# Kernel optimization log

Measured on AMD Instinct MI355X. Metric: run time of the kernel, lower is better.

The kernel has to match this reference:

```python
import jax, jax.numpy as jnp
import numpy as np

N_NODES = 100000
N_EDGES = 3200000
N_GRAPHS = 2000
IN_DIM = 12
HID = 48
ADME = 20
EPS = 1e-5


def setup_inputs() -> dict:
    key = jax.random.key(0)
    ks = jax.random.split(key, 24)
    x = jax.random.normal(ks[0], (N_NODES, IN_DIM), jnp.float32)
    edge_index = jax.random.randint(ks[1], (2, N_EDGES), 0, N_NODES, dtype=jnp.int64)
    batch = jnp.sort(jax.random.randint(ks[2], (N_NODES,), 0, N_GRAPHS, dtype=jnp.int64))
    adme = jax.random.normal(ks[3], (N_GRAPHS, ADME), jnp.float32)

    def lin(k, fo, fi):
        bound = 1.0 / np.sqrt(fi)
        return jax.random.uniform(k, (fo, fi), jnp.float32, -bound, bound)

    params = {
        # SAGEConv layer 0: lin_l (neighbors, with bias) and lin_r (root)
        'wl0': lin(ks[4], HID, IN_DIM), 'wr0': lin(ks[5], HID, IN_DIM),
        'bc0': jnp.zeros((HID,), jnp.float32),
        'g0': jnp.ones((HID,), jnp.float32), 'be0': jnp.zeros((HID,), jnp.float32),
        # SAGEConv layer 1
        'wl1': lin(ks[6], HID, HID), 'wr1': lin(ks[7], HID, HID),
        'bc1': jnp.zeros((HID,), jnp.float32),
        'g1': jnp.ones((HID,), jnp.float32), 'be1': jnp.zeros((HID,), jnp.float32),
        # head: Linear(116,64) -> BN -> ReLU -> Linear(64,32) -> ReLU -> Linear(32,1)
        'hw1': lin(ks[8], 64, 2 * HID + ADME), 'hb1': jnp.zeros((64,), jnp.float32),
        'hg1': jnp.ones((64,), jnp.float32), 'hbe1': jnp.zeros((64,), jnp.float32),
        'hw2': lin(ks[9], 32, 64), 'hb2': jnp.zeros((32,), jnp.float32),
        'hw3': lin(ks[10], 1, 32), 'hb3': jnp.zeros((1,), jnp.float32),
    }
    return dict(x=x, edge_index=edge_index, batch=batch, adme=adme, **params)


def _sage(x, src, dst, wl, wr, b):
    # mean-aggregate source features at destination nodes, then two linears
    msum = jax.ops.segment_sum(x[src], dst, num_segments=N_NODES)
    cnt = jax.ops.segment_sum(jnp.ones((src.shape[0],), x.dtype), dst, num_segments=N_NODES)
    agg = msum / jnp.maximum(cnt, 1.0)[:, None]
    return agg @ wl.T + x @ wr.T + b


def _bn(x, g, b):
    m = x.mean(0)
    v = x.var(0)  # biased variance (BatchNorm training-mode math)
    return g * (x - m) * jax.lax.rsqrt(v + EPS) + b


def reference(x, edge_index, batch, adme,
              wl0, wr0, bc0, g0, be0,
              wl1, wr1, bc1, g1, be1,
              hw1, hb1, hg1, hbe1, hw2, hb2, hw3, hb3):
    src, dst = edge_index[0], edge_index[1]
    # backbone (dropout is identity in eval)
    h = jax.nn.relu(_bn(_sage(x, src, dst, wl0, wr0, bc0), g0, be0))
    h = jax.nn.relu(_bn(_sage(h, src, dst, wl1, wr1, bc1), g1, be1))
    # global mean / max pools over graph ids
    s = jax.ops.segment_sum(h, batch, num_segments=N_GRAPHS)
    n = jax.ops.segment_sum(jnp.ones((h.shape[0],), h.dtype), batch, num_segments=N_GRAPHS)
    mean_p = s / jnp.maximum(n, 1.0)[:, None]
    max_p = jax.ops.segment_max(h, batch, num_segments=N_GRAPHS)
    max_p = jnp.where(n[:, None] > 0, max_p, 0.0)
    combined = jnp.concatenate([mean_p, max_p, adme], axis=-1)  # [B, 116]
    z = jax.nn.relu(_bn(combined @ hw1.T + hb1, hg1, hbe1))
    z = jax.nn.relu(z @ hw2.T + hb2)
    return (z @ hw3.T + hb3)[:, 0]
```

## Files before the change

kernel.cpp:

```cpp
#include <hip/hip_runtime.h>

#define NNODES  100000
#define NEDGES  3200000
#define NGRAPHS 2000
#define INDIM   12
#define HID     48
#define CEPS    1e-5f
#define CAP     96
#define SRCMID  (NNODES / 2)

#define BSHIFT   8
#define NBUCKET  ((NNODES + 255) / 256)
#define CAPB     8704
#define P1_BLOCKS 125
#define P1_EDGES (NEDGES / P1_BLOCKS)

#define SCAN_CHUNK 1024
#define NSCAN_BLOCKS ((NNODES + SCAN_CHUNK - 1) / SCAN_CHUNK)

__device__ inline void f4add(float4& a, const float4 b) {
  a.x += b.x; a.y += b.y; a.z += b.z; a.w += b.w;
}
__device__ inline float blo(unsigned u) { return __uint_as_float(u << 16); }
__device__ inline float bhi(unsigned u) { return __uint_as_float(u & 0xffff0000u); }
__device__ inline unsigned bpack(float a, float b) {
  unsigned ua = __float_as_uint(a), ub = __float_as_uint(b);
  ua = (ua + 0x7fffu + ((ua >> 16) & 1u)) >> 16;
  ub = (ub + 0x7fffu + ((ub >> 16) & 1u)) >> 16;
  return ua | (ub << 16);
}

__global__ __launch_bounds__(256) void convert_x_kernel(
    const float* __restrict__ x, uint4* __restrict__ xb) {
  int idx = blockIdx.x * blockDim.x + threadIdx.x;
  if (idx >= NNODES * INDIM / 8) return;
  const float4* p = (const float4*)(x + (size_t)idx * 8);
  float4 v0 = p[0], v1 = p[1];
  uint4 o;
  o.x = bpack(v0.x, v0.y); o.y = bpack(v0.z, v0.w);
  o.z = bpack(v1.x, v1.y); o.w = bpack(v1.z, v1.w);
  xb[idx] = o;
}

__global__ __launch_bounds__(256) void bucket_p1_kernel(
    const int* __restrict__ ei, int* __restrict__ bucket_cursor,
    unsigned int* __restrict__ bucketed) {
  __shared__ int hist[NBUCKET];
  __shared__ int lcur[NBUCKET];
  for (int b = threadIdx.x; b < NBUCKET; b += 256) hist[b] = 0;
  __syncthreads();
  const int base = blockIdx.x * P1_EDGES;
  for (int off = threadIdx.x * 4; off < P1_EDGES; off += 1024) {
    int4 d4 = *(const int4*)(ei + NEDGES + base + off);
    atomicAdd(&hist[(d4.x >> BSHIFT) % NBUCKET], 1);
    atomicAdd(&hist[(d4.y >> BSHIFT) % NBUCKET], 1);
    atomicAdd(&hist[(d4.z >> BSHIFT) % NBUCKET], 1);
    atomicAdd(&hist[(d4.w >> BSHIFT) % NBUCKET], 1);
  }
  __syncthreads();
  for (int b = threadIdx.x; b < NBUCKET; b += 256)
    lcur[b] = atomicAdd(&bucket_cursor[b], hist[b]);
  __syncthreads();
  for (int off = threadIdx.x * 4; off < P1_EDGES; off += 1024) {
    int4 s4 = *(const int4*)(ei + base + off);
    int4 d4 = *(const int4*)(ei + NEDGES + base + off);
    {
      int b0 = (d4.x >> BSHIFT) % NBUCKET; int p = atomicAdd(&lcur[b0], 1);
      if ((unsigned)p < (unsigned)CAPB)
        bucketed[(size_t)b0 * CAPB + p] = ((unsigned)(d4.x & 255) << 24) | ((unsigned)s4.x & 0xFFFFFFu);
    }
    {
      int b1 = (d4.y >> BSHIFT) % NBUCKET; int p = atomicAdd(&lcur[b1], 1);
      if ((unsigned)p < (unsigned)CAPB)
        bucketed[(size_t)b1 * CAPB + p] = ((unsigned)(d4.y & 255) << 24) | ((unsigned)s4.y & 0xFFFFFFu);
    }
    {
      int b2 = (d4.z >> BSHIFT) % NBUCKET; int p = atomicAdd(&lcur[b2], 1);
      if ((unsigned)p < (unsigned)CAPB)
        bucketed[(size_t)b2 * CAPB + p] = ((unsigned)(d4.z & 255) << 24) | ((unsigned)s4.z & 0xFFFFFFu);
    }
    {
      int b3 = (d4.w >> BSHIFT) % NBUCKET; int p = atomicAdd(&lcur[b3], 1);
      if ((unsigned)p < (unsigned)CAPB)
        bucketed[(size_t)b3 * CAPB + p] = ((unsigned)(d4.w & 255) << 24) | ((unsigned)s4.w & 0xFFFFFFu);
    }
  }
}

__global__ __launch_bounds__(256) void fill_p2_kernel(
    const unsigned int* __restrict__ bucketed, const int* __restrict__ bucket_cursor,
    int* __restrict__ slots, int* __restrict__ cnt) {
  __shared__ int clo[256], chi[256];
  clo[threadIdx.x] = 0; chi[threadIdx.x] = 0;
  __syncthreads();
  int b = blockIdx.x;
  int count = bucket_cursor[b];
  if (count > CAPB) count = CAPB;
  size_t bb = (size_t)b * CAPB;
  for (int i = threadIdx.x; i < count; i += 256) {
    unsigned v = bucketed[bb + i];
    int dl = (int)(v >> 24);
    int s = (int)(v & 0xFFFFFFu);
    int node = b * 256 + dl;
    if (node < NNODES) {
      if (s < SRCMID) {
        int p = atomicAdd(&clo[dl], 1);
        if ((unsigned)p < (unsigned)CAP) slots[(size_t)node * CAP + p] = s;
      } else {
        int p = atomicAdd(&chi[dl], 1);
        if ((unsigned)p < (unsigned)CAP) slots[(size_t)node * CAP + (CAP - 1 - p)] = s;
      }
    }
  }
  __syncthreads();
  int node = b * 256 + threadIdx.x;
  if (node < NNODES)
    cnt[node] = min(clo[threadIdx.x], CAP) | (min(chi[threadIdx.x], CAP) << 16);
}

__global__ __launch_bounds__(64) void graph_start_kernel(
    const int* __restrict__ batch, int* __restrict__ gstart) {
  int g = blockIdx.x * blockDim.x + threadIdx.x;
  if (g > NGRAPHS) return;
  int lo = 0, hi = NNODES;
  while (lo < hi) {
    int mid = (lo + hi) >> 1;
    if (batch[mid] < g) lo = mid + 1; else hi = mid;
  }
  gstart[g] = lo;
}

#define GATH24(BEGIN, COUNT)                                              \
  {                                                                       \
    int n = 0;                                                            \
    for (; n + 4 <= (COUNT); n += 4) {                                    \
      int sa = slots[(BEGIN) + n + 0];                                    \
      int sb = slots[(BEGIN) + n + 1];                                    \
      int sc = slots[(BEGIN) + n + 2];                                    \
      int sd = slots[(BEGIN) + n + 3];                                    \
      uint2 ua = xb[(size_t)sa * 3 + q];                                  \
      uint2 ub = xb[(size_t)sb * 3 + q];                                  \
      uint2 uc = xb[(size_t)sc * 3 + q];                                  \
      uint2 ud = xb[(size_t)sd * 3 + q];                                  \
      a0[0] += blo(ua.x); a0[1] += bhi(ua.x); a0[2] += blo(ua.y); a0[3] += bhi(ua.y); \
      a1[0] += blo(ub.x); a1[1] += bhi(ub.x); a1[2] += blo(ub.y); a1[3] += bhi(ub.y); \
      a2[0] += blo(uc.x); a2[1] += bhi(uc.x); a2[2] += blo(uc.y); a2[3] += bhi(uc.y); \
      a3[0] += blo(ud.x); a3[1] += bhi(ud.x); a3[2] += blo(ud.y); a3[3] += bhi(ud.y); \
    }                                                                     \
    for (; n < (COUNT); n++) {                                            \
      uint2 u = xb[(size_t)slots[(BEGIN) + n] * 3 + q];                   \
      a0[0] += blo(u.x); a0[1] += bhi(u.x); a0[2] += blo(u.y); a0[3] += bhi(u.y); \
    }                                                                     \
  }

__global__ __launch_bounds__(256) void agg0_b_kernel(
    const uint2* __restrict__ xb, const int* __restrict__ slots,
    const int* __restrict__ cnt, float* __restrict__ agg) {
  int tid = blockIdx.x * blockDim.x + threadIdx.x;
  int node = tid / 3;
  int q = tid - node * 3;
  if (node >= NNODES) return;
  size_t start = (size_t)node * CAP;
  int packed = cnt[node];
  int dlo = packed & 0xFFFF, dhi = packed >> 16;
  float a0[4] = {0,0,0,0}, a1[4] = {0,0,0,0}, a2[4] = {0,0,0,0}, a3[4] = {0,0,0,0};
  GATH24(start, dlo);
  GATH24(start + CAP - dhi, dhi);
  float inv = 1.0f / fmaxf((float)(dlo + dhi), 1.0f);
  float4 r;
  r.x = (a0[0] + a1[0] + a2[0] + a3[0]) * inv;
  r.y = (a0[1] + a1[1] + a2[1] + a3[1]) * inv;
  r.z = (a0[2] + a1[2] + a2[2] + a3[2]) * inv;
  r.w = (a0[3] + a1[3] + a2[3] + a3[3]) * inv;
  *(float4*)(agg + (size_t)node * INDIM + q * 4) = r;
}

__global__ __launch_bounds__(256) void sage0_4k_kernel(
    const float* __restrict__ x, const float* __restrict__ agg,
    const float* __restrict__ wl, const float* __restrict__ wr,
    const float* __restrict__ bc, float* __restrict__ hpre,
    float* __restrict__ stats) {
  __shared__ float swl[HID * INDIM], swr[HID * INDIM], sbc[HID];
  __shared__ float ssum[HID], ssq[HID];
  for (int t = threadIdx.x; t < HID * INDIM; t += 256) { swl[t] = wl[t]; swr[t] = wr[t]; }
  if (threadIdx.x < HID) {
    sbc[threadIdx.x] = bc[threadIdx.x];
    ssum[threadIdx.x] = 0.f; ssq[threadIdx.x] = 0.f;
  }
  __syncthreads();
  int tid = blockIdx.x * 256 + threadIdx.x;
  int node = tid >> 2;
  int kq = tid & 3;
  bool valid = (node < NNODES);
  float s[12], sq[12];
  if (valid) {
    float xi[INDIM], ag[INDIM];
    const float4* xp = (const float4*)(x + (size_t)node * INDIM);
    const float4* mp = (const float4*)(agg + (size_t)node * INDIM);
#pragma unroll
    for (int q = 0; q < 3; q++) {
      float4 v = xp[q];
      xi[q * 4 + 0] = v.x; xi[q * 4 + 1] = v.y; xi[q * 4 + 2] = v.z; xi[q * 4 + 3] = v.w;
      float4 m = mp[q];
      ag[q * 4 + 0] = m.x; ag[q * 4 + 1] = m.y; ag[q * 4 + 2] = m.z; ag[q * 4 + 3] = m.w;
    }
    float o[12];
#pragma unroll
    for (int t = 0; t < 12; t++) {
      int k = kq * 12 + t;
      const float* wlr = swl + k * INDIM;
      const float* wrr = swr + k * INDIM;
      float acc = sbc[k];
#pragma unroll
      for (int j = 0; j < INDIM; j++) acc += ag[j] * wlr[j] + xi[j] * wrr[j];
      o[t] = acc;
    }
    float* dst = hpre + (size_t)node * HID + kq * 12;
    *(float4*)(dst + 0) = make_float4(o[0], o[1], o[2], o[3]);
    *(float4*)(dst + 4) = make_float4(o[4], o[5], o[6], o[7]);
    *(float4*)(dst + 8) = make_float4(o[8], o[9], o[10], o[11]);
#pragma unroll
    for (int t = 0; t < 12; t++) { s[t] = o[t]; sq[t] = o[t] * o[t]; }
  } else {
#pragma unroll
    for (int t = 0; t < 12; t++) { s[t] = 0.f; sq[t] = 0.f; }
  }
#pragma unroll
  for (int off = 4; off <= 32; off <<= 1) {
#pragma unroll
    for (int t = 0; t < 12; t++) {
      s[t] += __shfl_xor(s[t], off);
      sq[t] += __shfl_xor(sq[t], off);
    }
  }
  int lane = threadIdx.x & 63;
  if (lane < 4) {
#pragma unroll
    for (int t = 0; t < 12; t++) {
      atomicAdd(&ssum[lane * 12 + t], s[t]);
      atomicAdd(&ssq[lane * 12 + t], sq[t]);
    }
  }
  __syncthreads();
  if (threadIdx.x < 2 * HID)
    atomicAdd(&stats[threadIdx.x],
              threadIdx.x < HID ? ssum[threadIdx.x] : ssq[threadIdx.x - HID]);
}

__global__ __launch_bounds__(256) void bn_relu_b16_kernel(
    const float* __restrict__ hpre, const float* __restrict__ stats,
    const float* __restrict__ g, const float* __restrict__ be,
    uint4* __restrict__ h0b) {
  __shared__ float sc[HID], sh[HID];
  if (threadIdx.x < HID) {
    int k = threadIdx.x;
    float m = stats[k] * (1.0f / NNODES);
    float v = stats[HID + k] * (1.0f / NNODES) - m * m;
    float s = g[k] * rsqrtf(v + CEPS);
    sc[k] = s; sh[k] = be[k] - m * s;
  }
  __syncthreads();
  int idx = blockIdx.x * 256 + threadIdx.x;
  if (idx >= NNODES * 6) return;
  const float4* p = (const float4*)(hpre + (size_t)idx * 8);
  float4 v0 = p[0], v1 = p[1];
  int kb = (idx % 6) * 8;
  float r0 = fmaxf(v0.x * sc[kb + 0] + sh[kb + 0], 0.f);
  float r1 = fmaxf(v0.y * sc[kb + 1] + sh[kb + 1], 0.f);
  float r2 = fmaxf(v0.z * sc[kb + 2] + sh[kb + 2], 0.f);
  float r3 = fmaxf(v0.w * sc[kb + 3] + sh[kb + 3], 0.f);
  float r4 = fmaxf(v1.x * sc[kb + 4] + sh[kb + 4], 0.f);
  float r5 = fmaxf(v1.y * sc[kb + 5] + sh[kb + 5], 0.f);
  float r6 = fmaxf(v1.z * sc[kb + 6] + sh[kb + 6], 0.f);
  float r7 = fmaxf(v1.w * sc[kb + 7] + sh[kb + 7], 0.f);
  uint4 o;
  o.x = bpack(r0, r1); o.y = bpack(r2, r3); o.z = bpack(r4, r5); o.w = bpack(r6, r7);
  h0b[idx] = o;
}

#define GATH48(BEGIN, COUNT)                                              \
  {                                                                       \
    int n = 0;                                                            \
    for (; n + 4 <= (COUNT); n += 4) {                                    \
      int sa = slots[(BEGIN) + n + 0];                                    \
      int sb = slots[(BEGIN) + n + 1];                                    \
      int sc = slots[(BEGIN) + n + 2];                                    \
      int sd = slots[(BEGIN) + n + 3];                                    \
      uint4 ua = h0b[(size_t)sa * 6 + q];                                 \
      uint4 ub = h0b[(size_t)sb * 6 + q];                                 \
      uint4 uc = h0b[(size_t)sc * 6 + q];                                 \
      uint4 ud = h0b[(size_t)sd * 6 + q];                                 \
      a0[0] += blo(ua.x); a0[1] += bhi(ua.x); a0[2] += blo(ua.y); a0[3] += bhi(ua.y); \
      a0[4] += blo(ua.z); a0[5] += bhi(ua.z); a0[6] += blo(ua.w); a0[7] += bhi(ua.w); \
      a1[0] += blo(ub.x); a1[1] += bhi(ub.x); a1[2] += blo(ub.y); a1[3] += bhi(ub.y); \
      a1[4] += blo(ub.z); a1[5] += bhi(ub.z); a1[6] += blo(ub.w); a1[7] += bhi(ub.w); \
      a2[0] += blo(uc.x); a2[1] += bhi(uc.x); a2[2] += blo(uc.y); a2[3] += bhi(uc.y); \
      a2[4] += blo(uc.z); a2[5] += bhi(uc.z); a2[6] += blo(uc.w); a2[7] += bhi(uc.w); \
      a3[0] += blo(ud.x); a3[1] += bhi(ud.x); a3[2] += blo(ud.y); a3[3] += bhi(ud.y); \
      a3[4] += blo(ud.z); a3[5] += bhi(ud.z); a3[6] += blo(ud.w); a3[7] += bhi(ud.w); \
    }                                                                     \
    for (; n < (COUNT); n++) {                                            \
      uint4 u = h0b[(size_t)slots[(BEGIN) + n] * 6 + q];                  \
      a0[0] += blo(u.x); a0[1] += bhi(u.x); a0[2] += blo(u.y); a0[3] += bhi(u.y); \
      a0[4] += blo(u.z); a0[5] += bhi(u.z); a0[6] += blo(u.w); a0[7] += bhi(u.w); \
    }                                                                     \
  }

__global__ __launch_bounds__(256) void agg1_b_kernel(
    const uint4* __restrict__ h0b, const int* __restrict__ slots,
    const int* __restrict__ cnt, float* __restrict__ agg) {
  int tid = blockIdx.x * blockDim.x + threadIdx.x;
  int node = tid / 6;
  int q = tid - node * 6;
  if (node >= NNODES) return;
  size_t start = (size_t)node * CAP;
  int packed = cnt[node];
  int dlo = packed & 0xFFFF, dhi = packed >> 16;
  float a0[8] = {0,0,0,0,0,0,0,0}, a1[8] = {0,0,0,0,0,0,0,0};
  float a2[8] = {0,0,0,0,0,0,0,0}, a3[8] = {0,0,0,0,0,0,0,0};
  GATH48(start, dlo);
  GATH48(start + CAP - dhi, dhi);
  float inv = 1.0f / fmaxf((float)(dlo + dhi), 1.0f);
  float* dst = agg + (size_t)node * HID + q * 8;
  float4 r0, r1;
  r0.x = (a0[0] + a1[0] + a2[0] + a3[0]) * inv;
  r0.y = (a0[1] + a1[1] + a2[1] + a3[1]) * inv;
  r0.z = (a0[2] + a1[2] + a2[2] + a3[2]) * inv;
  r0.w = (a0[3] + a1[3] + a2[3] + a3[3]) * inv;
  r1.x = (a0[4] + a1[4] + a2[4] + a3[4]) * inv;
  r1.y = (a0[5] + a1[5] + a2[5] + a3[5]) * inv;
  r1.z = (a0[6] + a1[6] + a2[6] + a3[6]) * inv;
  r1.w = (a0[7] + a1[7] + a2[7] + a3[7]) * inv;
  *(float4*)(dst + 0) = r0;
  *(float4*)(dst + 4) = r1;
}

__global__ __launch_bounds__(256) void sage1_2n_kernel(
    const float* __restrict__ agg, const uint2* __restrict__ h0b,
    const float* __restrict__ wl, const float* __restrict__ wr,
    const float* __restrict__ bc, float* __restrict__ hout,
    float* __restrict__ stats) {
  __shared__ float swl[HID * HID], swr[HID * HID], sbc[HID];
  __shared__ float ssum[HID], ssq[HID];
  for (int t = threadIdx.x; t < HID * HID; t += 256) { swl[t] = wl[t]; swr[t] = wr[t]; }
  if (threadIdx.x < HID) {
    sbc[threadIdx.x] = bc[threadIdx.x];
    ssum[threadIdx.x] = 0.f; ssq[threadIdx.x] = 0.f;
  }
  __syncthreads();
  int tid = blockIdx.x * 256 + threadIdx.x;
  int p = tid >> 2;
  int jq = tid & 3;
  bool valid = (p < NNODES / 2);
  const int jb = jq * 12;
  float s[12], sq[12];
  if (valid) {
    int node0 = 2 * p, node1 = 2 * p + 1;
    float a0[12], a1[12], h0v[12], h1v[12];
    const float4* ap0 = (const float4*)(agg + (size_t)node0 * HID + jb);
    const float4* ap1 = (const float4*)(agg + (size_t)node1 * HID + jb);
#pragma unroll
    for (int q = 0; q < 3; q++) {
      float4 v = ap0[q];
      a0[q * 4 + 0] = v.x; a0[q * 4 + 1] = v.y; a0[q * 4 + 2] = v.z; a0[q * 4 + 3] = v.w;
      float4 w = ap1[q];
      a1[q * 4 + 0] = w.x; a1[q * 4 + 1] = w.y; a1[q * 4 + 2] = w.z; a1[q * 4 + 3] = w.w;
    }
    const uint2* hp0 = h0b + (size_t)node0 * 12 + jq * 3;
    const uint2* hp1 = h0b + (size_t)node1 * 12 + jq * 3;
#pragma unroll
    for (int q = 0; q < 3; q++) {
      uint2 u = hp0[q];
      h0v[q * 4 + 0] = blo(u.x); h0v[q * 4 + 1] = bhi(u.x);
      h0v[q * 4 + 2] = blo(u.y); h0v[q * 4 + 3] = bhi(u.y);
      uint2 w = hp1[q];
      h1v[q * 4 + 0] = blo(w.x); h1v[q * 4 + 1] = bhi(w.x);
      h1v[q * 4 + 2] = blo(w.y); h1v[q * 4 + 3] = bhi(w.y);
    }
    float o0[12], o1[12];
#pragma unroll
    for (int k = 0; k < HID; k++) {
      const float* wlr = swl + k * HID + jb;
      const float* wrr = swr + k * HID + jb;
      float s0 = 0.f, s1 = 0.f;
#pragma unroll
      for (int j = 0; j < 12; j++) {
        float wlv = wlr[j], wrv = wrr[j];
        s0 += a0[j] * wlv + h0v[j] * wrv;
        s1 += a1[j] * wlv + h1v[j] * wrv;
      }
      s0 += __shfl_xor(s0, 1); s0 += __shfl_xor(s0, 2);
      s1 += __shfl_xor(s1, 1); s1 += __shfl_xor(s1, 2);
      if (jq == (k / 12)) {
        o0[k % 12] = s0 + sbc[k];
        o1[k % 12] = s1 + sbc[k];
      }
    }
    int node0b = node0, node1b = node1;
    float* d0 = hout + (size_t)node0b * HID + jb;
    float* d1 = hout + (size_t)node1b * HID + jb;
    *(float4*)(d0 + 0) = make_float4(o0[0], o0[1], o0[2], o0[3]);
    *(float4*)(d0 + 4) = make_float4(o0[4], o0[5], o0[6], o0[7]);
    *(float4*)(d0 + 8) = make_float4(o0[8], o0[9], o0[10], o0[11]);
    *(float4*)(d1 + 0) = make_float4(o1[0], o1[1], o1[2], o1[3]);
    *(float4*)(d1 + 4) = make_float4(o1[4], o1[5], o1[6], o1[7]);
    *(float4*)(d1 + 8) = make_float4(o1[8], o1[9], o1[10], o1[11]);
#pragma unroll
    for (int t = 0; t < 12; t++) {
      s[t] = o0[t] + o1[t];
      sq[t] = o0[t] * o0[t] + o1[t] * o1[t];
    }
  } else {
#pragma unroll
    for (int t = 0; t < 12; t++) { s[t] = 0.f; sq[t] = 0.f; }
  }
#pragma unroll
  for (int off = 4; off <= 32; off <<= 1) {
#pragma unroll
    for (int t = 0; t < 12; t++) {
      s[t] += __shfl_xor(s[t], off);
      sq[t] += __shfl_xor(sq[t], off);
    }
  }
  int lane = threadIdx.x & 63;
  if (lane < 4) {
#pragma unroll
    for (int t = 0; t < 12; t++) {
      atomicAdd(&ssum[lane * 12 + t], s[t]);
      atomicAdd(&ssq[lane * 12 + t], sq[t]);
    }
  }
  __syncthreads();
  if (threadIdx.x < 2 * HID)
    atomicAdd(&stats[threadIdx.x],
              threadIdx.x < HID ? ssum[threadIdx.x] : ssq[threadIdx.x - HID]);
}

__global__ __launch_bounds__(256) void bn_pool_kernel(
    const float* __restrict__ hpre, const float* __restrict__ stats,
    const float* __restrict__ g, const float* __restrict__ be,
    const int* __restrict__ gstart,
    float* __restrict__ meanp, float* __restrict__ maxp) {
  __shared__ float sum_s[4][HID], max_s[4][HID];
  int gr = blockIdx.x;
  int w = threadIdx.x >> 6;
  int f = threadIdx.x & 63;
  int start = gstart[gr], end = gstart[gr + 1];
  if (f < HID) {
    float m = stats[f] * (1.0f / NNODES);
    float v = stats[HID + f] * (1.0f / NNODES) - m * m;
    float sc = g[f] * rsqrtf(v + CEPS);
    float sh = be[f] - m * sc;
    float sum = 0.f, mx = 0.f;
    for (int i = start + w; i < end; i += 4) {
      float val = fmaxf(hpre[(size_t)i * HID + f] * sc + sh, 0.f);
      sum += val;
      mx = fmaxf(mx, val);
    }
    sum_s[w][f] = sum;
    max_s[w][f] = mx;
  }
  __syncthreads();
  if (threadIdx.x < HID) {
    int k = threadIdx.x;
    float s = sum_s[0][k] + sum_s[1][k] + sum_s[2][k] + sum_s[3][k];
    float mx = fmaxf(fmaxf(max_s[0][k], max_s[1][k]), fmaxf(max_s[2][k], max_s[3][k]));
    float n = (float)(end - start);
    meanp[(size_t)gr * HID + k] = s / fmaxf(n, 1.0f);
    maxp[(size_t)gr * HID + k] = mx;
  }
}

__global__ __launch_bounds__(64) void head1_kernel(
    const float* __restrict__ meanp, const float* __restrict__ maxp,
    const float* __restrict__ adme,
    const float* __restrict__ hw1, const float* __restrict__ hb1,
    float* __restrict__ z1) {
  int g = blockIdx.x;
  int t = threadIdx.x;
  __shared__ float comb[2 * HID + 20];
  if (t < HID) {
    comb[t] = meanp[(size_t)g * HID + t];
    comb[HID + t] = maxp[(size_t)g * HID + t];
  }
  if (t < 20) comb[2 * HID + t] = adme[(size_t)g * 20 + t];
  __syncthreads();
  float acc = hb1[t];
#pragma unroll
  for (int j = 0; j < 2 * HID + 20; j++) acc += comb[j] * hw1[t * (2 * HID + 20) + j];
  z1[(size_t)g * 64 + t] = acc;
}

__global__ __launch_bounds__(256) void headstats_kernel(
    const float* __restrict__ z1, const float* __restrict__ hg,
    const float* __restrict__ hbe, float* __restrict__ hsc, float* __restrict__ hsh) {
  int k = blockIdx.x;
  float s = 0.f, q = 0.f;
  for (int i = threadIdx.x; i < NGRAPHS; i += blockDim.x) {
    float v = z1[(size_t)i * 64 + k];
    s += v; q += v * v;
  }
  __shared__ float ls[4], lq[4];
  int lane = threadIdx.x & 63, w = threadIdx.x >> 6;
#pragma unroll
  for (int off = 32; off; off >>= 1) { s += __shfl_xor(s, off); q += __shfl_xor(q, off); }
  if (lane == 0) { ls[w] = s; lq[w] = q; }
  __syncthreads();
  if (threadIdx.x == 0) {
    s = ls[0] + ls[1] + ls[2] + ls[3];
    q = lq[0] + lq[1] + lq[2] + lq[3];
    float m = s * (1.0f / NGRAPHS);
    float v = q * (1.0f / NGRAPHS) - m * m;
    float sc = hg[k] * rsqrtf(v + CEPS);
    hsc[k] = sc; hsh[k] = hbe[k] - m * sc;
  }
}

__global__ __launch_bounds__(256) void head2_kernel(
    const float* __restrict__ z1, const float* __restrict__ hsc,
    const float* __restrict__ hsh, const float* __restrict__ hw2,
    const float* __restrict__ hb2, const float* __restrict__ hw3,
    const float* __restrict__ hb3, float* __restrict__ out) {
  __shared__ float sw2[32 * 64], sb2[32], sw3[32], ssc[64], ssh[64], sb3;
  for (int t = threadIdx.x; t < 32 * 64; t += blockDim.x) sw2[t] = hw2[t];
  if (threadIdx.x < 32) { sb2[threadIdx.x] = hb2[threadIdx.x]; sw3[threadIdx.x] = hw3[threadIdx.x]; }
  if (threadIdx.x < 64) { ssc[threadIdx.x] = hsc[threadIdx.x]; ssh[threadIdx.x] = hsh[threadIdx.x]; }
  if (threadIdx.x == 0) sb3 = hb3[0];
  __syncthreads();
  int g = blockIdx.x * blockDim.x + threadIdx.x;
  if (g >= NGRAPHS) return;
  float z[64];
#pragma unroll
  for (int k = 0; k < 64; k++) z[k] = fmaxf(z1[(size_t)g * 64 + k] * ssc[k] + ssh[k], 0.f);
  float o = sb3;
  for (int m = 0; m < 32; m++) {
    float a = sb2[m];
#pragma unroll
    for (int k = 0; k < 64; k++) a += z[k] * sw2[m * 64 + k];
    o += fmaxf(a, 0.f) * sw3[m];
  }
  out[g] = o;
}

__global__ __launch_bounds__(256) void hist_kernel(
    const int* __restrict__ ei, int* __restrict__ cnt) {
  int t = blockIdx.x * blockDim.x + threadIdx.x;
  int e = t * 4;
  if (e >= NEDGES) return;
  int4 d4 = *(const int4*)(ei + NEDGES + e);
  atomicAdd(cnt + d4.x, 1);
  atomicAdd(cnt + d4.y, 1);
  atomicAdd(cnt + d4.z, 1);
  atomicAdd(cnt + d4.w, 1);
}

__global__ __launch_bounds__(256) void scan_bsum_kernel(
    const int* __restrict__ cnt, int* __restrict__ bsum) {
  __shared__ int s[256];
  int base = blockIdx.x * SCAN_CHUNK + threadIdx.x * 4;
  int t = 0;
#pragma unroll
  for (int k = 0; k < 4; k++) {
    int i = base + k;
    if (i < NNODES) t += cnt[i];
  }
  s[threadIdx.x] = t;
  __syncthreads();
  for (int off = 128; off; off >>= 1) {
    if (threadIdx.x < off) s[threadIdx.x] += s[threadIdx.x + off];
    __syncthreads();
  }
  if (threadIdx.x == 0) bsum[blockIdx.x] = s[0];
}

__global__ void scan_bsum_excl_kernel(int* __restrict__ bsum) {
  if (threadIdx.x == 0 && blockIdx.x == 0) {
    int acc = 0;
    for (int b = 0; b < NSCAN_BLOCKS; b++) {
      int v = bsum[b];
      bsum[b] = acc;
      acc += v;
    }
  }
}

__global__ __launch_bounds__(256) void scan_final_kernel(
    const int* __restrict__ cnt, const int* __restrict__ bsum,
    int* __restrict__ row_ptr, int* __restrict__ cursor) {
  __shared__ int s[256];
  int base = blockIdx.x * SCAN_CHUNK + threadIdx.x * 4;
  int c[4];
  int tsum = 0;
#pragma unroll
  for (int k = 0; k < 4; k++) {
    int i = base + k;
    c[k] = (i < NNODES) ? cnt[i] : 0;
    tsum += c[k];
  }
  s[threadIdx.x] = tsum;
  __syncthreads();
  for (int off = 1; off < 256; off <<= 1) {
    int x = 0;
    if (threadIdx.x >= off) x = s[threadIdx.x - off];
    __syncthreads();
    s[threadIdx.x] += x;
    __syncthreads();
  }
  int running = bsum[blockIdx.x] + s[threadIdx.x] - tsum;
#pragma unroll
  for (int k = 0; k < 4; k++) {
    int i = base + k;
    if (i < NNODES) {
      row_ptr[i] = running;
      cursor[i] = running;
      running += c[k];
    }
  }
}

__global__ __launch_bounds__(256) void fill_kernel(
    const int* __restrict__ ei, int* __restrict__ cursor,
    int* __restrict__ sorted_src) {
  int t = blockIdx.x * blockDim.x + threadIdx.x;
  int e = t * 4;
  if (e >= NEDGES) return;
  int4 s4 = *(const int4*)(ei + e);
  int4 d4 = *(const int4*)(ei + NEDGES + e);
  int p0 = atomicAdd(cursor + d4.x, 1);
  int p1 = atomicAdd(cursor + d4.y, 1);
  int p2 = atomicAdd(cursor + d4.z, 1);
  int p3 = atomicAdd(cursor + d4.w, 1);
  sorted_src[p0] = s4.x;
  sorted_src[p1] = s4.y;
  sorted_src[p2] = s4.z;
  sorted_src[p3] = s4.w;
}

__global__ __launch_bounds__(256) void agg0f_kernel(
    const float* __restrict__ x, const int* __restrict__ slots,
    const int* __restrict__ row_ptr, const int* __restrict__ cnt,
    float* __restrict__ agg) {
  int tid = blockIdx.x * blockDim.x + threadIdx.x;
  int node = tid / 3;
  int q = tid - node * 3;
  if (node >= NNODES) return;
  int start = row_ptr[node];
  int deg = cnt[node];
  float4 a0 = {0,0,0,0};
  for (int n = 0; n < deg; n++)
    f4add(a0, *(const float4*)(x + (size_t)slots[start + n] * INDIM + q * 4));
  float inv = 1.0f / fmaxf((float)deg, 1.0f);
  float4 r; r.x = a0.x * inv; r.y = a0.y * inv; r.z = a0.z * inv; r.w = a0.w * inv;
  *(float4*)(agg + (size_t)node * INDIM + q * 4) = r;
}

__global__ __launch_bounds__(256) void agg1f_kernel(
    const float* __restrict__ h0, const int* __restrict__ slots,
    const int* __restrict__ row_ptr, const int* __restrict__ cnt,
    float* __restrict__ agg) {
  int tid = blockIdx.x * blockDim.x + threadIdx.x;
  int node = tid / 12;
  int q = tid - node * 12;
  if (node >= NNODES) return;
  int start = row_ptr[node];
  int deg = cnt[node];
  float4 a0 = {0,0,0,0};
  for (int n = 0; n < deg; n++)
    f4add(a0, *(const float4*)(h0 + (size_t)slots[start + n] * HID + q * 4));
  float inv = 1.0f / fmaxf((float)deg, 1.0f);
  float4 r; r.x = a0.x * inv; r.y = a0.y * inv; r.z = a0.z * inv; r.w = a0.w * inv;
  *(float4*)(agg + (size_t)node * HID + q * 4) = r;
}

__global__ __launch_bounds__(256) void sage0_kernel(
    const float* __restrict__ x, const float* __restrict__ agg,
    const float* __restrict__ wl, const float* __restrict__ wr,
    const float* __restrict__ bc,
    float* __restrict__ hpre, float* __restrict__ stats) {
  __shared__ float swl[HID * INDIM], swr[HID * INDIM], sbc[HID];
  __shared__ float ssum[HID], ssq[HID];
  for (int t = threadIdx.x; t < HID * INDIM; t += blockDim.x) { swl[t] = wl[t]; swr[t] = wr[t]; }
  if (threadIdx.x < HID) { sbc[threadIdx.x] = bc[threadIdx.x]; ssum[threadIdx.x] = 0.f; ssq[threadIdx.x] = 0.f; }
  __syncthreads();
  int i = blockIdx.x * blockDim.x + threadIdx.x;
  bool valid = (i < NNODES);
  float xi[INDIM], ag[INDIM];
  if (valid) {
    const float4* xp = (const float4*)(x + (size_t)i * INDIM);
    const float4* mp = (const float4*)(agg + (size_t)i * INDIM);
#pragma unroll
    for (int q = 0; q < 3; q++) {
      float4 v = xp[q];
      xi[q * 4 + 0] = v.x; xi[q * 4 + 1] = v.y; xi[q * 4 + 2] = v.z; xi[q * 4 + 3] = v.w;
      float4 m = mp[q];
      ag[q * 4 + 0] = m.x; ag[q * 4 + 1] = m.y; ag[q * 4 + 2] = m.z; ag[q * 4 + 3] = m.w;
    }
  } else {
#pragma unroll
    for (int j = 0; j < INDIM; j++) { xi[j] = 0.f; ag[j] = 0.f; }
  }
  int lane = threadIdx.x & 63;
  for (int kb = 0; kb < HID; kb += 4) {
    float o[4];
#pragma unroll
    for (int t = 0; t < 4; t++) {
      int k = kb + t;
      float acc = valid ? sbc[k] : 0.f;
#pragma unroll
      for (int j = 0; j < INDIM; j++)
        acc += ag[j] * swl[k * INDIM + j] + xi[j] * swr[k * INDIM + j];
      o[t] = acc;
    }
    if (valid) {
      float4 v; v.x = o[0]; v.y = o[1]; v.z = o[2]; v.w = o[3];
      *((float4*)(hpre + (size_t)i * HID + kb)) = v;
    }
#pragma unroll
    for (int t = 0; t < 4; t++) {
      float s = o[t], q = o[t] * o[t];
#pragma unroll
      for (int off = 32; off; off >>= 1) { s += __shfl_xor(s, off); q += __shfl_xor(q, off); }
      if (lane == 0) { atomicAdd(&ssum[kb + t], s); atomicAdd(&ssq[kb + t], q); }
    }
  }
  __syncthreads();
  if (threadIdx.x < HID) {
    atomicAdd(&stats[threadIdx.x], ssum[threadIdx.x]);
    atomicAdd(&stats[HID + threadIdx.x], ssq[threadIdx.x]);
  }
}

__global__ __launch_bounds__(256) void bn_relu_kernel(
    float* __restrict__ h, const float* __restrict__ stats,
    const float* __restrict__ g, const float* __restrict__ be) {
  __shared__ float sc[HID], sh[HID];
  if (threadIdx.x < HID) {
    int k = threadIdx.x;
    float m = stats[k] * (1.0f / NNODES);
    float v = stats[HID + k] * (1.0f / NNODES) - m * m;
    float s = g[k] * rsqrtf(v + CEPS);
    sc[k] = s; sh[k] = be[k] - m * s;
  }
  __syncthreads();
  const int total = NNODES * (HID / 4);
  int stride = gridDim.x * blockDim.x;
  for (int idx = blockIdx.x * blockDim.x + threadIdx.x; idx < total; idx += stride) {
    int kb = (idx % (HID / 4)) * 4;
    float4 v = ((float4*)h)[idx];
    v.x = fmaxf(v.x * sc[kb + 0] + sh[kb + 0], 0.f);
    v.y = fmaxf(v.y * sc[kb + 1] + sh[kb + 1], 0.f);
    v.z = fmaxf(v.z * sc[kb + 2] + sh[kb + 2], 0.f);
    v.w = fmaxf(v.w * sc[kb + 3] + sh[kb + 3], 0.f);
    ((float4*)h)[idx] = v;
  }
}

__global__ __launch_bounds__(256) void sage1_kernel(
    const float* __restrict__ h0, float* __restrict__ agg_hpre,
    const float* __restrict__ wl, const float* __restrict__ wr,
    const float* __restrict__ bc, float* __restrict__ stats) {
  __shared__ float swl[HID * HID], swr[HID * HID], sbc[HID];
  __shared__ float ssum[HID], ssq[HID];
  for (int t = threadIdx.x; t < HID * HID; t += blockDim.x) { swl[t] = wl[t]; swr[t] = wr[t]; }
  if (threadIdx.x < HID) { sbc[threadIdx.x] = bc[threadIdx.x]; ssum[threadIdx.x] = 0.f; ssq[threadIdx.x] = 0.f; }
  __syncthreads();
  int i = blockIdx.x * blockDim.x + threadIdx.x;
  bool valid = (i < NNODES);
  float ag[HID], hx[HID];
  if (valid) {
    const float4* mp = (const float4*)(agg_hpre + (size_t)i * HID);
    const float4* hp = (const float4*)(h0 + (size_t)i * HID);
#pragma unroll
    for (int q = 0; q < HID / 4; q++) {
      float4 m = mp[q];
      ag[q * 4 + 0] = m.x; ag[q * 4 + 1] = m.y; ag[q * 4 + 2] = m.z; ag[q * 4 + 3] = m.w;
      float4 v = hp[q];
      hx[q * 4 + 0] = v.x; hx[q * 4 + 1] = v.y; hx[q * 4 + 2] = v.z; hx[q * 4 + 3] = v.w;
    }
  } else {
#pragma unroll
    for (int j = 0; j < HID; j++) { ag[j] = 0.f; hx[j] = 0.f; }
  }
  int lane = threadIdx.x & 63;
  for (int kb = 0; kb < HID; kb += 4) {
    float o[4];
#pragma unroll
    for (int t = 0; t < 4; t++) {
      int k = kb + t;
      float acc = valid ? sbc[k] : 0.f;
#pragma unroll
      for (int j = 0; j < HID; j++)
        acc += ag[j] * swl[k * HID + j] + hx[j] * swr[k * HID + j];
      o[t] = acc;
    }
    if (valid) {
      float4 v; v.x = o[0]; v.y = o[1]; v.z = o[2]; v.w = o[3];
      *((float4*)(agg_hpre + (size_t)i * HID + kb)) = v;
    }
#pragma unroll
    for (int t = 0; t < 4; t++) {
      float s = o[t], q = o[t] * o[t];
#pragma unroll
      for (int off = 32; off; off >>= 1) { s += __shfl_xor(s, off); q += __shfl_xor(q, off); }
      if (lane == 0) { atomicAdd(&ssum[kb + t], s); atomicAdd(&ssq[kb + t], q); }
    }
  }
  __syncthreads();
  if (threadIdx.x < HID) {
    atomicAdd(&stats[threadIdx.x], ssum[threadIdx.x]);
    atomicAdd(&stats[HID + threadIdx.x], ssq[threadIdx.x]);
  }
}

__global__ __launch_bounds__(64) void bn_pool1w_kernel(
    const float* __restrict__ hpre, const float* __restrict__ stats,
    const float* __restrict__ g, const float* __restrict__ be,
    const int* __restrict__ gstart,
    float* __restrict__ meanp, float* __restrict__ maxp) {
  int gr = blockIdx.x;
  int f = threadIdx.x;
  if (f >= HID) return;
  float m = stats[f] * (1.0f / NNODES);
  float v = stats[HID + f] * (1.0f / NNODES) - m * m;
  float sc = g[f] * rsqrtf(v + CEPS);
  float sh = be[f] - m * sc;
  int start = gstart[gr], end = gstart[gr + 1];
  float sum = 0.f, mx = 0.f;
  for (int i = start; i < end; i++) {
    float val = fmaxf(hpre[(size_t)i * HID + f] * sc + sh, 0.f);
    sum += val;
    mx = fmaxf(mx, val);
  }
  float n = (float)(end - start);
  meanp[(size_t)gr * HID + f] = sum / fmaxf(n, 1.0f);
  maxp[(size_t)gr * HID + f] = mx;
}

extern "C" void kernel_launch(void* const* d_in, const int* in_sizes, int n_in,
                              void* d_out, int out_size, void* d_ws, size_t ws_size,
                              hipStream_t stream) {
  (void)in_sizes; (void)n_in; (void)out_size;
  const float* x     = (const float*)d_in[0];
  const int*   ei    = (const int*)d_in[1];
  const int*   batch = (const int*)d_in[2];
  const float* adme  = (const float*)d_in[3];
  const float* wl0 = (const float*)d_in[4];
  const float* wr0 = (const float*)d_in[5];
  const float* bc0 = (const float*)d_in[6];
  const float* g0  = (const float*)d_in[7];
  const float* be0 = (const float*)d_in[8];
  const float* wl1 = (const float*)d_in[9];
  const float* wr1 = (const float*)d_in[10];
  const float* bc1 = (const float*)d_in[11];
  const float* g1  = (const float*)d_in[12];
  const float* be1 = (const float*)d_in[13];
  const float* hw1 = (const float*)d_in[14];
  const float* hb1 = (const float*)d_in[15];
  const float* hg1 = (const float*)d_in[16];
  const float* hbe1= (const float*)d_in[17];
  const float* hw2 = (const float*)d_in[18];
  const float* hb2 = (const float*)d_in[19];
  const float* hw3 = (const float*)d_in[20];
  const float* hb3 = (const float*)d_in[21];
  float* out = (float*)d_out;

  size_t elems_A = (size_t)NNODES * HID * 2 + (size_t)NNODES * CAP + 2048
                 + 512 + NNODES + 4 * HID
                 + (size_t)NGRAPHS * HID * 2 + (size_t)NGRAPHS * 64 + 128;
  bool padded = ws_size >= elems_A * 4 + 256;

  if (padded) {
    float* buf1 = (float*)d_ws;
    float* buf2 = buf1 + (size_t)NNODES * HID;
    int* slots  = (int*)(buf2 + (size_t)NNODES * HID);
    int* gstart = slots + (size_t)NNODES * CAP;
    int* bucket_cursor = gstart + 2048;
    int* cnt    = bucket_cursor + 512;
    float* stats0 = (float*)(cnt + NNODES);
    float* stats1 = stats0 + 2 * HID;
    float* meanp = stats1 + 2 * HID;
    float* maxp  = meanp + (size_t)NGRAPHS * HID;
    float* z1  = maxp + (size_t)NGRAPHS * HID;
    float* hsc = z1 + (size_t)NGRAPHS * 64;
    float* hsh = hsc + 64;

    unsigned int* bucketed = (unsigned int*)buf2;
    uint4* h0b = (uint4*)buf1;
    uint2* xb  = (uint2*)(buf1 + 4200000);

    hipMemsetAsync(bucket_cursor, 0, 512 * sizeof(int), stream);
    hipMemsetAsync(stats0, 0, 4 * HID * sizeof(float), stream);

    convert_x_kernel<<<(NNODES * INDIM / 8 + 255) / 256, 256, 0, stream>>>(x, (uint4*)xb);
    bucket_p1_kernel<<<P1_BLOCKS, 256, 0, stream>>>(ei, bucket_cursor, bucketed);
    fill_p2_kernel<<<NBUCKET, 256, 0, stream>>>(bucketed, bucket_cursor, slots, cnt);
    graph_start_kernel<<<(NGRAPHS + 1 + 63) / 64, 64, 0, stream>>>(batch, gstart);

    agg0_b_kernel<<<(NNODES * 3 + 255) / 256, 256, 0, stream>>>(xb, slots, cnt, buf1);
    sage0_4k_kernel<<<(NNODES * 4 + 255) / 256, 256, 0, stream>>>(x, buf1, wl0, wr0, bc0, buf2, stats0);
    bn_relu_b16_kernel<<<(NNODES * 6 + 255) / 256, 256, 0, stream>>>(buf2, stats0, g0, be0, h0b);

    agg1_b_kernel<<<(NNODES * 6 + 255) / 256, 256, 0, stream>>>(h0b, slots, cnt, buf2);
    sage1_2n_kernel<<<(NNODES * 2 + 255) / 256, 256, 0, stream>>>(buf2, (const uint2*)h0b, wl1, wr1, bc1, buf2, stats1);
    bn_pool_kernel<<<NGRAPHS, 256, 0, stream>>>(buf2, stats1, g1, be1, gstart, meanp, maxp);

    head1_kernel<<<NGRAPHS, 64, 0, stream>>>(meanp, maxp, adme, hw1, hb1, z1);
    headstats_kernel<<<64, 256, 0, stream>>>(z1, hg1, hbe1, hsc, hsh);
    head2_kernel<<<(NGRAPHS + 255) / 256, 256, 0, stream>>>(z1, hsc, hsh, hw2, hb2, hw3, hb3, out);
  } else {
    float* buf1 = (float*)d_ws;
    float* buf2 = buf1 + (size_t)NNODES * HID;
    int* sorted_src = (int*)(buf2 + (size_t)NNODES * HID);
    int* row_ptr = sorted_src + NEDGES;
    int* cursor  = row_ptr + NNODES;
    int* bsum    = cursor + NNODES;
    int* gstart  = bsum + 128;
    int* cnt   = gstart + 2048;
    float* stats0 = (float*)(cnt + NNODES);
    float* stats1 = stats0 + 2 * HID;
    float* meanp = stats1 + 2 * HID;
    float* maxp  = meanp + (size_t)NGRAPHS * HID;
    float* z1  = maxp + (size_t)NGRAPHS * HID;
    float* hsc = z1 + (size_t)NGRAPHS * 64;
    float* hsh = hsc + 64;

    size_t zero_bytes = (char*)(stats1 + 2 * HID) - (char*)cnt;
    hipMemsetAsync(cnt, 0, zero_bytes, stream);

    hist_kernel<<<(NEDGES / 4 + 255) / 256, 256, 0, stream>>>(ei, cnt);
    scan_bsum_kernel<<<NSCAN_BLOCKS, 256, 0, stream>>>(cnt, bsum);
    scan_bsum_excl_kernel<<<1, 64, 0, stream>>>(bsum);
    scan_final_kernel<<<NSCAN_BLOCKS, 256, 0, stream>>>(cnt, bsum, row_ptr, cursor);
    fill_kernel<<<(NEDGES / 4 + 255) / 256, 256, 0, stream>>>(ei, cursor, sorted_src);
    graph_start_kernel<<<(NGRAPHS + 1 + 63) / 64, 64, 0, stream>>>(batch, gstart);

    agg0f_kernel<<<(NNODES * 3 + 255) / 256, 256, 0, stream>>>(x, sorted_src, row_ptr, cnt, buf1);
    sage0_kernel<<<(NNODES + 255) / 256, 256, 0, stream>>>(x, buf1, wl0, wr0, bc0, buf2, stats0);
    bn_relu_kernel<<<2048, 256, 0, stream>>>(buf2, stats0, g0, be0);

    agg1f_kernel<<<(NNODES * 12 + 255) / 256, 256, 0, stream>>>(buf2, sorted_src, row_ptr, cnt, buf1);
    sage1_kernel<<<(NNODES + 255) / 256, 256, 0, stream>>>(buf2, buf1, wl1, wr1, bc1, stats1);
    bn_pool1w_kernel<<<NGRAPHS, 64, 0, stream>>>(buf1, stats1, g1, be1, gstart, meanp, maxp);

    head1_kernel<<<NGRAPHS, 64, 0, stream>>>(meanp, maxp, adme, hw1, hb1, z1);
    headstats_kernel<<<64, 256, 0, stream>>>(z1, hg1, hbe1, hsc, hsh);
    head2_kernel<<<(NGRAPHS + 255) / 256, 256, 0, stream>>>(z1, hsc, hsh, hw2, hb2, hw3, hb3, out);
  }
}
```

Before: 288.4 us.

## Sort per-node neighbor slots into eight source-range groups for gather locality

The fill kernel now does a two-pass counting sort of each node's incoming sources into eight contiguous source-id ranges, replacing the old two-way low/high split. Neighbour lists become roughly ordered by source id, so concurrent gathers across nodes touch nearby feature rows, and the aggregation loops shrink to a single contiguous segment. The bucketing pass also uses five times as many blocks and skips global atomics for empty buckets. In exchange, the fill kernel reads the bucketed edges twice and uses more shared memory.

```diff
diff --git a/kernel.cpp b/kernel.cpp
--- a/kernel.cpp
+++ b/kernel.cpp
@@ -7,13 +7,13 @@
 #define HID     48
 #define CEPS    1e-5f
 #define CAP     96
-#define SRCMID  (NNODES / 2)
 
 #define BSHIFT   8
 #define NBUCKET  ((NNODES + 255) / 256)
 #define CAPB     8704
-#define P1_BLOCKS 125
+#define P1_BLOCKS 625
 #define P1_EDGES (NEDGES / P1_BLOCKS)
+#define NGRP     8
 
 #define SCAN_CHUNK 1024
 #define NSCAN_BLOCKS ((NNODES + SCAN_CHUNK - 1) / SCAN_CHUNK)
@@ -59,7 +59,7 @@
   }
   __syncthreads();
   for (int b = threadIdx.x; b < NBUCKET; b += 256)
-    lcur[b] = atomicAdd(&bucket_cursor[b], hist[b]);
+    lcur[b] = (hist[b] > 0) ? atomicAdd(&bucket_cursor[b], hist[b]) : 0;
   __syncthreads();
   for (int off = threadIdx.x * 4; off < P1_EDGES; off += 1024) {
     int4 s4 = *(const int4*)(ei + base + off);
@@ -90,8 +90,10 @@
 __global__ __launch_bounds__(256) void fill_p2_kernel(
     const unsigned int* __restrict__ bucketed, const int* __restrict__ bucket_cursor,
     int* __restrict__ slots, int* __restrict__ cnt) {
-  __shared__ int clo[256], chi[256];
-  clo[threadIdx.x] = 0; chi[threadIdx.x] = 0;
+  __shared__ int cbase[256][NGRP];
+  __shared__ int ccur[256][NGRP];
+#pragma unroll
+  for (int g = 0; g < NGRP; g++) { cbase[threadIdx.x][g] = 0; ccur[threadIdx.x][g] = 0; }
   __syncthreads();
   int b = blockIdx.x;
   int count = bucket_cursor[b];
@@ -100,22 +102,34 @@
   for (int i = threadIdx.x; i < count; i += 256) {
     unsigned v = bucketed[bb + i];
     int dl = (int)(v >> 24);
+    int g = (int)((v & 0xFFFFFFu) >> 14);
+    atomicAdd(&cbase[dl][g], 1);
+  }
+  __syncthreads();
+  {
+    int dl = threadIdx.x;
+    int run = 0;
+#pragma unroll
+    for (int g = 0; g < NGRP; g++) {
+      int c = cbase[dl][g];
+      cbase[dl][g] = (run < CAP) ? run : CAP;
+      run += c;
+    }
+    int node = b * 256 + dl;
+    if (node < NNODES) cnt[node] = min(run, CAP);
+  }
+  __syncthreads();
+  for (int i = threadIdx.x; i < count; i += 256) {
+    unsigned v = bucketed[bb + i];
+    int dl = (int)(v >> 24);
     int s = (int)(v & 0xFFFFFFu);
+    int g = s >> 14;
     int node = b * 256 + dl;
     if (node < NNODES) {
-      if (s < SRCMID) {
-        int p = atomicAdd(&clo[dl], 1);
-        if ((unsigned)p < (unsigned)CAP) slots[(size_t)node * CAP + p] = s;
-      } else {
-        int p = atomicAdd(&chi[dl], 1);
-        if ((unsigned)p < (unsigned)CAP) slots[(size_t)node * CAP + (CAP - 1 - p)] = s;
-      }
-    }
-  }
-  __syncthreads();
-  int node = b * 256 + threadIdx.x;
-  if (node < NNODES)
-    cnt[node] = min(clo[threadIdx.x], CAP) | (min(chi[threadIdx.x], CAP) << 16);
+      int p = cbase[dl][g] + atomicAdd(&ccur[dl][g], 1);
+      if (p < CAP) slots[(size_t)node * CAP + p] = s;
+    }
+  }
 }
 
 __global__ __launch_bounds__(64) void graph_start_kernel(
@@ -130,29 +144,6 @@
   gstart[g] = lo;
 }
 
-#define GATH24(BEGIN, COUNT)                                              \
-  {                                                                       \
-    int n = 0;                                                            \
-    for (; n + 4 <= (COUNT); n += 4) {                                    \
-      int sa = slots[(BEGIN) + n + 0];                                    \
-      int sb = slots[(BEGIN) + n + 1];                                    \
-      int sc = slots[(BEGIN) + n + 2];                                    \
-      int sd = slots[(BEGIN) + n + 3];                                    \
-      uint2 ua = xb[(size_t)sa * 3 + q];                                  \
-      uint2 ub = xb[(size_t)sb * 3 + q];                                  \
-      uint2 uc = xb[(size_t)sc * 3 + q];                                  \
-      uint2 ud = xb[(size_t)sd * 3 + q];                                  \
-      a0[0] += blo(ua.x); a0[1] += bhi(ua.x); a0[2] += blo(ua.y); a0[3] += bhi(ua.y); \
-      a1[0] += blo(ub.x); a1[1] += bhi(ub.x); a1[2] += blo(ub.y); a1[3] += bhi(ub.y); \
-      a2[0] += blo(uc.x); a2[1] += bhi(uc.x); a2[2] += blo(uc.y); a2[3] += bhi(uc.y); \
-      a3[0] += blo(ud.x); a3[1] += bhi(ud.x); a3[2] += blo(ud.y); a3[3] += bhi(ud.y); \
-    }                                                                     \
-    for (; n < (COUNT); n++) {                                            \
-      uint2 u = xb[(size_t)slots[(BEGIN) + n] * 3 + q];                   \
-      a0[0] += blo(u.x); a0[1] += bhi(u.x); a0[2] += blo(u.y); a0[3] += bhi(u.y); \
-    }                                                                     \
-  }
-
 __global__ __launch_bounds__(256) void agg0_b_kernel(
     const uint2* __restrict__ xb, const int* __restrict__ slots,
     const int* __restrict__ cnt, float* __restrict__ agg) {
@@ -161,12 +152,28 @@
   int q = tid - node * 3;
   if (node >= NNODES) return;
   size_t start = (size_t)node * CAP;
-  int packed = cnt[node];
-  int dlo = packed & 0xFFFF, dhi = packed >> 16;
+  int deg = cnt[node];
   float a0[4] = {0,0,0,0}, a1[4] = {0,0,0,0}, a2[4] = {0,0,0,0}, a3[4] = {0,0,0,0};
-  GATH24(start, dlo);
-  GATH24(start + CAP - dhi, dhi);
-  float inv = 1.0f / fmaxf((float)(dlo + dhi), 1.0f);
+  int n = 0;
+  for (; n + 4 <= deg; n += 4) {
+    int sa = slots[start + n + 0];
+    int sb = slots[start + n + 1];
+    int sc = slots[start + n + 2];
+    int sd = slots[start + n + 3];
+    uint2 ua = xb[(size_t)sa * 3 + q];
+    uint2 ub = xb[(size_t)sb * 3 + q];
+    uint2 uc = xb[(size_t)sc * 3 + q];
+    uint2 ud = xb[(size_t)sd * 3 + q];
+    a0[0] += blo(ua.x); a0[1] += bhi(ua.x); a0[2] += blo(ua.y); a0[3] += bhi(ua.y);
+    a1[0] += blo(ub.x); a1[1] += bhi(ub.x); a1[2] += blo(ub.y); a1[3] += bhi(ub.y);
+    a2[0] += blo(uc.x); a2[1] += bhi(uc.x); a2[2] += blo(uc.y); a2[3] += bhi(uc.y);
+    a3[0] += blo(ud.x); a3[1] += bhi(ud.x); a3[2] += blo(ud.y); a3[3] += bhi(ud.y);
+  }
+  for (; n < deg; n++) {
+    uint2 u = xb[(size_t)slots[start + n] * 3 + q];
+    a0[0] += blo(u.x); a0[1] += bhi(u.x); a0[2] += blo(u.y); a0[3] += bhi(u.y);
+  }
+  float inv = 1.0f / fmaxf((float)deg, 1.0f);
   float4 r;
   r.x = (a0[0] + a1[0] + a2[0] + a3[0]) * inv;
   r.y = (a0[1] + a1[1] + a2[1] + a3[1]) * inv;
@@ -278,34 +285,6 @@
   h0b[idx] = o;
 }
 
-#define GATH48(BEGIN, COUNT)                                              \
-  {                                                                       \
-    int n = 0;                                                            \
-    for (; n + 4 <= (COUNT); n += 4) {                                    \
-      int sa = slots[(BEGIN) + n + 0];                                    \
-      int sb = slots[(BEGIN) + n + 1];                                    \
-      int sc = slots[(BEGIN) + n + 2];                                    \
-      int sd = slots[(BEGIN) + n + 3];                                    \
-      uint4 ua = h0b[(size_t)sa * 6 + q];                                 \
-      uint4 ub = h0b[(size_t)sb * 6 + q];                                 \
-      uint4 uc = h0b[(size_t)sc * 6 + q];                                 \
-      uint4 ud = h0b[(size_t)sd * 6 + q];                                 \
-      a0[0] += blo(ua.x); a0[1] += bhi(ua.x); a0[2] += blo(ua.y); a0[3] += bhi(ua.y); \
-      a0[4] += blo(ua.z); a0[5] += bhi(ua.z); a0[6] += blo(ua.w); a0[7] += bhi(ua.w); \
-      a1[0] += blo(ub.x); a1[1] += bhi(ub.x); a1[2] += blo(ub.y); a1[3] += bhi(ub.y); \
-      a1[4] += blo(ub.z); a1[5] += bhi(ub.z); a1[6] += blo(ub.w); a1[7] += bhi(ub.w); \
-      a2[0] += blo(uc.x); a2[1] += bhi(uc.x); a2[2] += blo(uc.y); a2[3] += bhi(uc.y); \
-      a2[4] += blo(uc.z); a2[5] += bhi(uc.z); a2[6] += blo(uc.w); a2[7] += bhi(uc.w); \
-      a3[0] += blo(ud.x); a3[1] += bhi(ud.x); a3[2] += blo(ud.y); a3[3] += bhi(ud.y); \
-      a3[4] += blo(ud.z); a3[5] += bhi(ud.z); a3[6] += blo(ud.w); a3[7] += bhi(ud.w); \
-    }                                                                     \
-    for (; n < (COUNT); n++) {                                            \
-      uint4 u = h0b[(size_t)slots[(BEGIN) + n] * 6 + q];                  \
-      a0[0] += blo(u.x); a0[1] += bhi(u.x); a0[2] += blo(u.y); a0[3] += bhi(u.y); \
-      a0[4] += blo(u.z); a0[5] += bhi(u.z); a0[6] += blo(u.w); a0[7] += bhi(u.w); \
-    }                                                                     \
-  }
-
 __global__ __launch_bounds__(256) void agg1_b_kernel(
     const uint4* __restrict__ h0b, const int* __restrict__ slots,
     const int* __restrict__ cnt, float* __restrict__ agg) {
@@ -314,13 +293,34 @@
   int q = tid - node * 6;
   if (node >= NNODES) return;
   size_t start = (size_t)node * CAP;
-  int packed = cnt[node];
-  int dlo = packed & 0xFFFF, dhi = packed >> 16;
+  int deg = cnt[node];
   float a0[8] = {0,0,0,0,0,0,0,0}, a1[8] = {0,0,0,0,0,0,0,0};
   float a2[8] = {0,0,0,0,0,0,0,0}, a3[8] = {0,0,0,0,0,0,0,0};
-  GATH48(start, dlo);
-  GATH48(start + CAP - dhi, dhi);
-  float inv = 1.0f / fmaxf((float)(dlo + dhi), 1.0f);
+  int n = 0;
+  for (; n + 4 <= deg; n += 4) {
+    int sa = slots[start + n + 0];
+    int sb = slots[start + n + 1];
+    int sc = slots[start + n + 2];
+    int sd = slots[start + n + 3];
+    uint4 ua = h0b[(size_t)sa * 6 + q];
+    uint4 ub = h0b[(size_t)sb * 6 + q];
+    uint4 uc = h0b[(size_t)sc * 6 + q];
+    uint4 ud = h0b[(size_t)sd * 6 + q];
+    a0[0] += blo(ua.x); a0[1] += bhi(ua.x); a0[2] += blo(ua.y); a0[3] += bhi(ua.y);
+    a0[4] += blo(ua.z); a0[5] += bhi(ua.z); a0[6] += blo(ua.w); a0[7] += bhi(ua.w);
+    a1[0] += blo(ub.x); a1[1] += bhi(ub.x); a1[2] += blo(ub.y); a1[3] += bhi(ub.y);
+    a1[4] += blo(ub.z); a1[5] += bhi(ub.z); a1[6] += blo(ub.w); a1[7] += bhi(ub.w);
+    a2[0] += blo(uc.x); a2[1] += bhi(uc.x); a2[2] += blo(uc.y); a2[3] += bhi(uc.y);
+    a2[4] += blo(uc.z); a2[5] += bhi(uc.z); a2[6] += blo(uc.w); a2[7] += bhi(uc.w);
+    a3[0] += blo(ud.x); a3[1] += bhi(ud.x); a3[2] += blo(ud.y); a3[3] += bhi(ud.y);
+    a3[4] += blo(ud.z); a3[5] += bhi(ud.z); a3[6] += blo(ud.w); a3[7] += bhi(ud.w);
+  }
+  for (; n < deg; n++) {
+    uint4 u = h0b[(size_t)slots[start + n] * 6 + q];
+    a0[0] += blo(u.x); a0[1] += bhi(u.x); a0[2] += blo(u.y); a0[3] += bhi(u.y);
+    a0[4] += blo(u.z); a0[5] += bhi(u.z); a0[6] += blo(u.w); a0[7] += bhi(u.w);
+  }
+  float inv = 1.0f / fmaxf((float)deg, 1.0f);
   float* dst = agg + (size_t)node * HID + q * 8;
   float4 r0, r1;
   r0.x = (a0[0] + a1[0] + a2[0] + a3[0]) * inv;
@@ -396,9 +396,8 @@
         o1[k % 12] = s1 + sbc[k];
       }
     }
-    int node0b = node0, node1b = node1;
-    float* d0 = hout + (size_t)node0b * HID + jb;
-    float* d1 = hout + (size_t)node1b * HID + jb;
+    float* d0 = hout + (size_t)node0 * HID + jb;
+    float* d1 = hout + (size_t)node1 * HID + jb;
     *(float4*)(d0 + 0) = make_float4(o0[0], o0[1], o0[2], o0[3]);
     *(float4*)(d0 + 4) = make_float4(o0[4], o0[5], o0[6], o0[7]);
     *(float4*)(d0 + 8) = make_float4(o0[8], o0[9], o0[10], o0[11]);
```

Result: slower. 297.7 us (+3.2%).
